# Optimization experiments

Hardware: AMD Instinct MI355X
Metric: run time of the kernel (lower is better)

## Reference

```python
import jax, jax.numpy as jnp
import numpy as np

EMB = 1024
HEAD = 128

def setup_inputs() -> dict:
    key = jax.random.key(0)
    ks = jax.random.split(key, 7)
    B, S = 4, 4096
    x = jax.random.normal(ks[0], (B, S, EMB), dtype=jnp.float32)
    s_in = 1.0 / np.sqrt(EMB)
    Wq = jax.random.uniform(ks[1], (EMB, HEAD), jnp.float32, -s_in, s_in)
    bq = jax.random.uniform(ks[2], (HEAD,), jnp.float32, -s_in, s_in)
    Wk = jax.random.uniform(ks[3], (EMB, HEAD), jnp.float32, -s_in, s_in)
    bk = jax.random.uniform(ks[4], (HEAD,), jnp.float32, -s_in, s_in)
    Wv = jax.random.uniform(ks[5], (EMB, HEAD), jnp.float32, -s_in, s_in)
    bv = jax.random.uniform(ks[6], (HEAD,), jnp.float32, -s_in, s_in)
    return {"decoder_sequence": x, "Wq": Wq, "bq": bq, "Wk": Wk, "bk": bk, "Wv": Wv, "bv": bv}

def reference(decoder_sequence, Wq, bq, Wk, bk, Wv, bv):
    # QKV projections: [B,S,E] @ [E,H] -> [B,S,H]
    Q = decoder_sequence @ Wq + bq
    K = decoder_sequence @ Wk + bk
    V = decoder_sequence @ Wv + bv
    S = decoder_sequence.shape[1]
    scale = 1.0 / jnp.sqrt(jnp.asarray(HEAD, Q.dtype))
    # scores [B,S,S]
    A = jnp.einsum('bid,bjd->bij', Q, K) * scale
    causal = jnp.tril(jnp.ones((S, S), dtype=bool))  # keep lower-triangular incl. diag
    A = jnp.where(causal, A, -jnp.inf)
    A = jax.nn.softmax(A, axis=-1)
    return jnp.einsum('bij,bjd->bid', A, V)
```

## Files before the change

kernel.cpp:

```cpp
#include <hip/hip_runtime.h>
#include <hip/hip_bf16.h>
#include <math.h>

#define S_LEN 4096
#define EMB   1024
#define HEAD  128

typedef short bf16x8 __attribute__((ext_vector_type(8)));
typedef short s16x4  __attribute__((ext_vector_type(4)));
typedef float f32x4  __attribute__((ext_vector_type(4)));

static __device__ __forceinline__ short f2bf(float x){
  unsigned u = __builtin_bit_cast(unsigned, x);
  u += 0x7fffu + ((u >> 16) & 1u);
  return (short)(u >> 16);
}
static __device__ __forceinline__ float bf2f(short s){
  unsigned u = ((unsigned)(unsigned short)s) << 16;
  return __builtin_bit_cast(float, u);
}
static __device__ __forceinline__ f32x4 mfma16(bf16x8 a, bf16x8 b, f32x4 c){
  return __builtin_amdgcn_mfma_f32_16x16x32_bf16(a, b, c, 0, 0, 0);
}
static __device__ __forceinline__ void gload16(const void* g, void* l){
  __builtin_amdgcn_global_load_lds((const __attribute__((address_space(1))) unsigned*)g,
                                   (__attribute__((address_space(3))) unsigned*)l, 16, 0, 0);
}

__global__ void prep_w(const float* __restrict__ Wq, const float* __restrict__ bq,
                       const float* __restrict__ Wk, const float* __restrict__ bk,
                       const float* __restrict__ Wv, const float* __restrict__ bv,
                       short* __restrict__ WT, float* __restrict__ bias){
  int idx = blockIdx.x * 256 + threadIdx.x;
  int nc  = idx >> 10;
  int k   = idx & 1023;
  int mat = nc >> 7;
  int n   = nc & 127;
  const float* W = (mat == 0) ? Wq : (mat == 1) ? Wk : Wv;
  float s = (mat == 0) ? 0.08838834764831845f : 1.0f;
  WT[idx] = f2bf(W[k * HEAD + n] * s);
  if (idx < 384){
    int m2 = idx >> 7, n2 = idx & 127;
    const float* bsrc = (m2 == 0) ? bq : (m2 == 1) ? bk : bv;
    float s2 = (m2 == 0) ? 0.08838834764831845f : 1.0f;
    bias[idx] = bsrc[n2] * s2;
  }
}

__global__ __launch_bounds__(1024) void qkv_proj(const float* __restrict__ x,
    const short* __restrict__ WT, const float* __restrict__ bias,
    short* __restrict__ Qo, short* __restrict__ Ko, short* __restrict__ VTo){
  __shared__ __align__(16) short Sm[2][32768];

  const int tid = threadIdx.x;
  const int wave = tid >> 6, lane = tid & 63, lr = lane & 15, hg = lane >> 4;
  const int wrg = wave >> 3, cg = wave & 7, fbase = cg * 3;
  const int row0 = blockIdx.x * 64;

  const f32x4 zero = {0.f, 0.f, 0.f, 0.f};
  f32x4 acc[2][3];
  #pragma unroll
  for (int rf = 0; rf < 2; ++rf)
    #pragma unroll
    for (int f = 0; f < 3; ++f) acc[rf][f] = zero;

#define WL(buf) (&Sm[buf][0])
#define XL(buf) ((float*)&Sm[buf][24576])

#define QKV_STAGE(buf, k0)                                                         \
  {                                                                                \
    _Pragma("unroll")                                                              \
    for (int s = 0; s < 3; ++s){                                                   \
      int slot = s * 16 + wave;                                                    \
      int ff = slot >> 1, ks = slot & 1;                                           \
      gload16(WT + (size_t)(ff * 16 + lr) * 1024 + (k0) + ks * 32 + hg * 8,        \
              WL(buf) + slot * 512);                                               \
    }                                                                              \
    {                                                                              \
      int rr = wave * 4 + hg;                                                      \
      int cs = lr ^ (rr & 15);                                                     \
      gload16(x + (size_t)(row0 + rr) * 1024 + (k0) + cs * 4,                      \
              XL(buf) + wave * 256);                                               \
    }                                                                              \
  }

  QKV_STAGE(0, 0)

  int cur = 0;
  for (int t = 0; t < 16; ++t){
    if (t < 15){
      QKV_STAGE(cur ^ 1, (t + 1) * 64)
      asm volatile("s_waitcnt vmcnt(4)" ::: "memory");
    } else {
      asm volatile("s_waitcnt vmcnt(0)" ::: "memory");
    }
    __builtin_amdgcn_s_barrier();
    asm volatile("" ::: "memory");

    bf16x8 a[2][2];
    #pragma unroll
    for (int rf = 0; rf < 2; ++rf){
      const int xr = wrg * 32 + rf * 16 + lr;
      #pragma unroll
      for (int ks = 0; ks < 2; ++ks){
        int s0 = ks * 8 + hg * 2;
        f32x4 xa = *(const f32x4*)&XL(cur)[xr * 64 + ((s0 ^ lr) << 2)];
        f32x4 xb = *(const f32x4*)&XL(cur)[xr * 64 + (((s0 + 1) ^ lr) << 2)];
        a[rf][ks][0] = f2bf(xa[0]); a[rf][ks][1] = f2bf(xa[1]);
        a[rf][ks][2] = f2bf(xa[2]); a[rf][ks][3] = f2bf(xa[3]);
        a[rf][ks][4] = f2bf(xb[0]); a[rf][ks][5] = f2bf(xb[1]);
        a[rf][ks][6] = f2bf(xb[2]); a[rf][ks][7] = f2bf(xb[3]);
      }
    }
    __builtin_amdgcn_s_setprio(1);
    #pragma unroll
    for (int fi = 0; fi < 3; ++fi){
      #pragma unroll
      for (int ks = 0; ks < 2; ++ks){
        bf16x8 bfr = *(const bf16x8*)&WL(cur)[((fbase + fi) * 2 + ks) * 512 + lane * 8];
        acc[0][fi] = mfma16(a[0][ks], bfr, acc[0][fi]);
        acc[1][fi] = mfma16(a[1][ks], bfr, acc[1][fi]);
      }
    }
    __builtin_amdgcn_s_setprio(0);
    asm volatile("" ::: "memory");
    __builtin_amdgcn_s_barrier();
    cur ^= 1;
  }

  short* Vb = &Sm[0][0];
  #pragma unroll
  for (int rf = 0; rf < 2; ++rf){
    #pragma unroll
    for (int fi = 0; fi < 3; ++fi){
      int f = fbase + fi;
      float bb = bias[f * 16 + lr];
      int rloc = wrg * 32 + rf * 16 + hg * 4;
      if (f < 16){
        short* dst = (f < 8) ? Qo : Ko;
        int col = (f & 7) * 16 + lr;
        #pragma unroll
        for (int r = 0; r < 4; ++r)
          dst[(size_t)(row0 + rloc + r) * HEAD + col] = f2bf(acc[rf][fi][r] + bb);
      } else {
        int vcol = (f - 16) * 16 + lr;
        #pragma unroll
        for (int r = 0; r < 4; ++r)
          Vb[vcol * 72 + rloc + r] = f2bf(acc[rf][fi][r] + bb);
      }
    }
  }
  __syncthreads();
  {
    int vcol = tid >> 3, sq = tid & 7;
    bf16x8 v = *(const bf16x8*)&Vb[vcol * 72 + sq * 8];
    int bb2 = row0 >> 12, ss = row0 & 4095;
    *(bf16x8*)(VTo + ((size_t)(bb2 * HEAD + vcol)) * S_LEN + ss + sq * 8) = v;
  }
}

#define PPS 36

__global__ __launch_bounds__(128, 2) void attn(const short* __restrict__ Q,
    const short* __restrict__ K, const short* __restrict__ VT,
    short* __restrict__ Opart, float* __restrict__ ML){
  __shared__ __align__(16) short Kl[2][4096];
  __shared__ __align__(16) short Vl[2][4096];
  __shared__ __align__(16) short Pl[2][2][16 * PPS];

  const int tid = threadIdx.x;
  const int wave = tid >> 6, lane = tid & 63, lr = lane & 15, hg = lane >> 4;
  const int b = blockIdx.x;
  const int i = blockIdx.y;

  int t, c;
  if (i < 232){
    c = 0;
    #pragma unroll
    for (int j = 1; j < 8; ++j) if (i >= j * (61 - 4 * j)) c = j;
    t = 8 * c + 7 + (i - c * (61 - 4 * c));
  } else {
    int p = i - 232;
    t = p + p / 7;
    c = t >> 3;
  }

  const int qt0  = t * 64;
  const int kvlo = c << 9;
  const int kvhi = min(kvlo + 512, qt0 + 64);
  const int ns   = (kvhi - kvlo) >> 5;

  const short* Qg = Q  + ((size_t)b * S_LEN + qt0 + wave * 32) * HEAD;
  const short* Kg = K  + (size_t)b * S_LEN * HEAD;
  const short* Vg = VT + (size_t)b * HEAD * S_LEN;

  bf16x8 qf[2][4];
  #pragma unroll
  for (int qs = 0; qs < 2; ++qs)
    #pragma unroll
    for (int sl = 0; sl < 4; ++sl)
      qf[qs][sl] = *(const bf16x8*)(Qg + (size_t)(qs * 16 + lr) * HEAD + sl * 32 + hg * 8);

#define ATTN_STAGE(buf, j0)                                                        \
  {                                                                                \
    if (wave == 0){                                                                \
      _Pragma("unroll")                                                            \
      for (int s = 0; s < 8; ++s)                                                  \
        gload16(Kg + (size_t)((j0) + (s >> 2) * 16 + lr) * HEAD + (s & 3) * 32 + hg * 8, \
                &Kl[buf][s * 512]);                                                \
    } else {                                                                       \
      _Pragma("unroll")                                                            \
      for (int s = 0; s < 8; ++s)                                                  \
        gload16(Vg + (size_t)(s * 16 + lr) * S_LEN + (j0) + hg * 8,                \
                &Vl[buf][s * 512]);                                                \
    }                                                                              \
  }

  ATTN_STAGE(0, kvlo)

  const f32x4 zero = {0.f, 0.f, 0.f, 0.f};
  f32x4 acc[8][2];
  #pragma unroll
  for (int f = 0; f < 8; ++f){ acc[f][0] = zero; acc[f][1] = zero; }
  float mloc[2] = {-INFINITY, -INFINITY};
  float den[2]  = {0.f, 0.f};

  int cur = 0;
  for (int st = 0; st < ns; ++st){
    const int j0 = kvlo + st * 32;
    if (st + 1 < ns){
      ATTN_STAGE(cur ^ 1, j0 + 32)
      asm volatile("s_waitcnt vmcnt(8)" ::: "memory");
    } else {
      asm volatile("s_waitcnt vmcnt(0)" ::: "memory");
    }
    __builtin_amdgcn_s_barrier();
    asm volatile("" ::: "memory");

    f32x4 sc[2][2];
    __builtin_amdgcn_s_setprio(1);
    #pragma unroll
    for (int kvs = 0; kvs < 2; ++kvs){
      sc[kvs][0] = zero; sc[kvs][1] = zero;
      #pragma unroll
      for (int sl = 0; sl < 4; ++sl){
        bf16x8 kf = *(const bf16x8*)&Kl[cur][(kvs * 4 + sl) * 512 + lane * 8];
        sc[kvs][0] = mfma16(kf, qf[0][sl], sc[kvs][0]);
        sc[kvs][1] = mfma16(kf, qf[1][sl], sc[kvs][1]);
      }
    }
    __builtin_amdgcn_s_setprio(0);

    if (j0 + 31 > qt0 + wave * 32){
      #pragma unroll
      for (int qs = 0; qs < 2; ++qs){
        int qr0 = qt0 + wave * 32 + qs * 16;
        #pragma unroll
        for (int kvs = 0; kvs < 2; ++kvs){
          int kv0 = j0 + kvs * 16 + hg * 4;
          #pragma unroll
          for (int r = 0; r < 4; ++r)
            if (kv0 + r > qr0 + lr) sc[kvs][qs][r] = -INFINITY;
        }
      }
    }

    float pm[2];
    #pragma unroll
    for (int qs = 0; qs < 2; ++qs){
      pm[qs] = fmaxf(fmaxf(fmaxf(sc[0][qs][0], sc[0][qs][1]), fmaxf(sc[0][qs][2], sc[0][qs][3])),
                     fmaxf(fmaxf(sc[1][qs][0], sc[1][qs][1]), fmaxf(sc[1][qs][2], sc[1][qs][3])));
      pm[qs] = fmaxf(pm[qs], __shfl_xor(pm[qs], 16));
      pm[qs] = fmaxf(pm[qs], __shfl_xor(pm[qs], 32));
    }

    if (__any(fmaxf(pm[0] - mloc[0], pm[1] - mloc[1]) > 8.0f)){
      #pragma unroll
      for (int qs = 0; qs < 2; ++qs){
        float mn = fmaxf(mloc[qs], pm[qs]);
        float al = __expf(mloc[qs] - mn);
        mloc[qs] = mn; den[qs] *= al;
        #pragma unroll
        for (int f = 0; f < 8; ++f) acc[f][qs] *= al;
      }
    }

    bf16x8 pf[2];
    #pragma unroll
    for (int qs = 0; qs < 2; ++qs){
      float rs = 0.f;
      s16x4 pb0, pb1;
      #pragma unroll
      for (int r = 0; r < 4; ++r){
        float p0 = __expf(sc[0][qs][r] - mloc[qs]);
        float p1 = __expf(sc[1][qs][r] - mloc[qs]);
        rs += p0 + p1;
        pb0[r] = f2bf(p0); pb1[r] = f2bf(p1);
      }
      rs += __shfl_xor(rs, 16);
      rs += __shfl_xor(rs, 32);
      den[qs] += rs;
      short* Pw = &Pl[wave][qs][0];
      *(s16x4*)(&Pw[lr * PPS + hg * 4])      = pb0;
      *(s16x4*)(&Pw[lr * PPS + 16 + hg * 4]) = pb1;
      pf[qs] = *(const bf16x8*)(&Pw[lr * PPS + hg * 8]);
    }

    __builtin_amdgcn_s_setprio(1);
    #pragma unroll
    for (int f = 0; f < 8; ++f){
      bf16x8 vf = *(const bf16x8*)&Vl[cur][f * 512 + lane * 8];
      acc[f][0] = mfma16(vf, pf[0], acc[f][0]);
      acc[f][1] = mfma16(vf, pf[1], acc[f][1]);
    }
    __builtin_amdgcn_s_setprio(0);

    asm volatile("" ::: "memory");
    __builtin_amdgcn_s_barrier();
    cur ^= 1;
  }

  const int pidx = b * 288 + i;
  short* Op = Opart + (size_t)pidx * 8192;
  #pragma unroll
  for (int qs = 0; qs < 2; ++qs){
    const float inv = 1.0f / den[qs];
    const int rowblk = wave * 2 + qs;
    #pragma unroll
    for (int f = 0; f < 8; ++f){
      s16x4 ov;
      #pragma unroll
      for (int r = 0; r < 4; ++r) ov[r] = f2bf(acc[f][qs][r] * inv);
      *(s16x4*)(Op + (rowblk * 16 + lr) * 128 + f * 16 + hg * 4) = ov;
    }
    if (hg == 0){
      ML[pidx * 128 + rowblk * 16 + lr]      = mloc[qs];
      ML[pidx * 128 + 64 + rowblk * 16 + lr] = den[qs];
    }
  }
}

__global__ __launch_bounds__(512) void combine(const short* __restrict__ Opart,
    const float* __restrict__ ML, float* __restrict__ out){
  const int t = blockIdx.x, b = blockIdx.y;
  const int row = threadIdx.x >> 3;
  const int cgp = threadIdx.x & 7;
  const int nc = (t >> 3) + 1;
  const int nheavy = (t + 1) >> 3;

  float M = -INFINITY;
  for (int cc = 0; cc < nc; ++cc){
    int ii = (cc < nheavy) ? cc * (61 - 4 * cc) + t - (8 * cc + 7)
                           : 232 + t - (t >> 3);
    M = fmaxf(M, ML[(b * 288 + ii) * 128 + row]);
  }
  float L = 0.f;
  float o[16];
  #pragma unroll
  for (int e = 0; e < 16; ++e) o[e] = 0.f;
  for (int cc = 0; cc < nc; ++cc){
    int ii = (cc < nheavy) ? cc * (61 - 4 * cc) + t - (8 * cc + 7)
                           : 232 + t - (t >> 3);
    int id = b * 288 + ii;
    float mc = ML[id * 128 + row];
    float lc = ML[id * 128 + 64 + row];
    float w = __expf(mc - M) * lc;
    L += w;
    const short* op = Opart + (size_t)id * 8192 + row * 128 + cgp * 16;
    bf16x8 v0 = *(const bf16x8*)(op);
    bf16x8 v1 = *(const bf16x8*)(op + 8);
    #pragma unroll
    for (int e = 0; e < 8; ++e){
      o[e]     += w * bf2f(v0[e]);
      o[8 + e] += w * bf2f(v1[e]);
    }
  }
  float inv = 1.f / L;
  float* dst = out + ((size_t)b * S_LEN + t * 64 + row) * HEAD + cgp * 16;
  #pragma unroll
  for (int e4 = 0; e4 < 4; ++e4){
    float4 w4 = { o[e4*4]*inv, o[e4*4+1]*inv, o[e4*4+2]*inv, o[e4*4+3]*inv };
    *(float4*)(dst + e4 * 4) = w4;
  }
}

extern "C" void kernel_launch(void* const* d_in, const int* in_sizes, int n_in,
                              void* d_out, int out_size, void* d_ws, size_t ws_size,
                              hipStream_t stream){
  const float* x  = (const float*)d_in[0];
  const float* Wq = (const float*)d_in[1];
  const float* bq = (const float*)d_in[2];
  const float* Wk = (const float*)d_in[3];
  const float* bk = (const float*)d_in[4];
  const float* Wv = (const float*)d_in[5];
  const float* bv = (const float*)d_in[6];
  float* out = (float*)d_out;

  char* ws = (char*)d_ws;
  short* WT    = (short*)(ws);
  float* bias  = (float*)(ws + 786432);
  short* Qb    = (short*)(ws + (1u << 20));
  short* Kb    = (short*)(ws + (1u << 20) + 4194304u);
  short* VTb   = (short*)(ws + (1u << 20) + 8388608u);
  short* Opart = (short*)(ws + 13631488u);
  float* ML    = (float*)(ws + 32505856u);

  prep_w<<<1536, 256, 0, stream>>>(Wq, bq, Wk, bk, Wv, bv, WT, bias);
  qkv_proj<<<256, 1024, 0, stream>>>(x, WT, bias, Qb, Kb, VTb);
  attn<<<dim3(4, 288), 128, 0, stream>>>(Qb, Kb, VTb, Opart, ML);
  combine<<<dim3(64, 4), 512, 0, stream>>>(Opart, ML, out);
}
```

Before: 105.4 us.

## Enlarge attention blocks to eight waves over 256-row query tiles

The attention kernel moves from 2-wave blocks covering 64 query rows to 8-wave blocks covering 256 query rows. All eight waves now share each staged K/V tile, and every wave issues one K load and one V load per stage. The split-KV work map is rebuilt around 512-key chunks with half-length diagonal blocks, and the partial-output layout and the combine kernel are re-indexed to match. This cuts global-to-LDS traffic per unit of work. The cost is far fewer blocks (288 on a 256-CU part) with uneven lengths, and coarser causal tiles that compute more masked entries on the diagonal.

```diff
diff --git a/kernel.cpp b/kernel.cpp
--- a/kernel.cpp
+++ b/kernel.cpp
@@ -161,34 +161,35 @@
 
 #define PPS 36
 
-__global__ __launch_bounds__(128, 2) void attn(const short* __restrict__ Q,
+__global__ __launch_bounds__(512) void attn(const short* __restrict__ Q,
     const short* __restrict__ K, const short* __restrict__ VT,
     short* __restrict__ Opart, float* __restrict__ ML){
   __shared__ __align__(16) short Kl[2][4096];
   __shared__ __align__(16) short Vl[2][4096];
-  __shared__ __align__(16) short Pl[2][2][16 * PPS];
+  __shared__ __align__(16) short Pl[8][16 * PPS];
 
   const int tid = threadIdx.x;
   const int wave = tid >> 6, lane = tid & 63, lr = lane & 15, hg = lane >> 4;
   const int b = blockIdx.x;
   const int i = blockIdx.y;
 
-  int t, c;
-  if (i < 232){
-    c = 0;
-    #pragma unroll
-    for (int j = 1; j < 8; ++j) if (i >= j * (61 - 4 * j)) c = j;
-    t = 8 * c + 7 + (i - c * (61 - 4 * c));
+  int t, c, full;
+  if (i < 64){
+    int acc = 0; t = 0; c = 0;
+    #pragma unroll
+    for (int tt = 0; tt < 16; ++tt){
+      int nf = (tt & 1) ? (tt >> 1) + 1 : (tt >> 1);
+      if (i >= acc && i < acc + nf){ t = tt; c = i - acc; }
+      acc += nf;
+    }
+    full = 1;
   } else {
-    int p = i - 232;
-    t = p + p / 7;
-    c = t >> 3;
-  }
-
-  const int qt0  = t * 64;
+    int k = i - 64; t = 2 * k; c = k; full = 0;
+  }
+
+  const int qt0  = t * 256;
   const int kvlo = c << 9;
-  const int kvhi = min(kvlo + 512, qt0 + 64);
-  const int ns   = (kvhi - kvlo) >> 5;
+  const int ns   = full ? 16 : 8;
 
   const short* Qg = Q  + ((size_t)b * S_LEN + qt0 + wave * 32) * HEAD;
   const short* Kg = K  + (size_t)b * S_LEN * HEAD;
@@ -203,17 +204,10 @@
 
 #define ATTN_STAGE(buf, j0)                                                        \
   {                                                                                \
-    if (wave == 0){                                                                \
-      _Pragma("unroll")                                                            \
-      for (int s = 0; s < 8; ++s)                                                  \
-        gload16(Kg + (size_t)((j0) + (s >> 2) * 16 + lr) * HEAD + (s & 3) * 32 + hg * 8, \
-                &Kl[buf][s * 512]);                                                \
-    } else {                                                                       \
-      _Pragma("unroll")                                                            \
-      for (int s = 0; s < 8; ++s)                                                  \
-        gload16(Vg + (size_t)(s * 16 + lr) * S_LEN + (j0) + hg * 8,                \
-                &Vl[buf][s * 512]);                                                \
-    }                                                                              \
+    gload16(Kg + (size_t)((j0) + (wave >> 2) * 16 + lr) * HEAD + (wave & 3) * 32 + hg * 8, \
+            &Kl[buf][wave * 512]);                                                 \
+    gload16(Vg + (size_t)(wave * 16 + lr) * S_LEN + (j0) + hg * 8,                 \
+            &Vl[buf][wave * 512]);                                                 \
   }
 
   ATTN_STAGE(0, kvlo)
@@ -230,7 +224,7 @@
     const int j0 = kvlo + st * 32;
     if (st + 1 < ns){
       ATTN_STAGE(cur ^ 1, j0 + 32)
-      asm volatile("s_waitcnt vmcnt(8)" ::: "memory");
+      asm volatile("s_waitcnt vmcnt(2)" ::: "memory");
     } else {
       asm volatile("s_waitcnt vmcnt(0)" ::: "memory");
     }
@@ -286,6 +280,7 @@
     }
 
     bf16x8 pf[2];
+    short* Pw = &Pl[wave][0];
     #pragma unroll
     for (int qs = 0; qs < 2; ++qs){
       float rs = 0.f;
@@ -300,7 +295,6 @@
       rs += __shfl_xor(rs, 16);
       rs += __shfl_xor(rs, 32);
       den[qs] += rs;
-      short* Pw = &Pl[wave][qs][0];
       *(s16x4*)(&Pw[lr * PPS + hg * 4])      = pb0;
       *(s16x4*)(&Pw[lr * PPS + 16 + hg * 4]) = pb1;
       pf[qs] = *(const bf16x8*)(&Pw[lr * PPS + hg * 8]);
@@ -320,53 +314,55 @@
     cur ^= 1;
   }
 
-  const int pidx = b * 288 + i;
-  short* Op = Opart + (size_t)pidx * 8192;
+  const int pidx = b * 72 + i;
+  short* Op = Opart + (size_t)pidx * 32768;
   #pragma unroll
   for (int qs = 0; qs < 2; ++qs){
     const float inv = 1.0f / den[qs];
-    const int rowblk = wave * 2 + qs;
+    const int rI = wave * 32 + qs * 16 + lr;
     #pragma unroll
     for (int f = 0; f < 8; ++f){
       s16x4 ov;
       #pragma unroll
       for (int r = 0; r < 4; ++r) ov[r] = f2bf(acc[f][qs][r] * inv);
-      *(s16x4*)(Op + (rowblk * 16 + lr) * 128 + f * 16 + hg * 4) = ov;
+      *(s16x4*)(Op + rI * 128 + f * 16 + hg * 4) = ov;
     }
     if (hg == 0){
-      ML[pidx * 128 + rowblk * 16 + lr]      = mloc[qs];
-      ML[pidx * 128 + 64 + rowblk * 16 + lr] = den[qs];
+      ML[pidx * 512 + rI]       = mloc[qs];
+      ML[pidx * 512 + 256 + rI] = den[qs];
     }
   }
 }
 
 __global__ __launch_bounds__(512) void combine(const short* __restrict__ Opart,
     const float* __restrict__ ML, float* __restrict__ out){
-  const int t = blockIdx.x, b = blockIdx.y;
+  const int bx = blockIdx.x, b = blockIdx.y;
+  const int t = bx >> 2, sub = bx & 3;
   const int row = threadIdx.x >> 3;
   const int cgp = threadIdx.x & 7;
-  const int nc = (t >> 3) + 1;
-  const int nheavy = (t + 1) >> 3;
+  const int rI = sub * 64 + row;
+  const int k = t >> 1;
+  const int F = k * k + ((t & 1) ? k : 0);
+  const int nf = (t & 1) ? k + 1 : k;
+  const int nc = k + 1;
 
   float M = -INFINITY;
   for (int cc = 0; cc < nc; ++cc){
-    int ii = (cc < nheavy) ? cc * (61 - 4 * cc) + t - (8 * cc + 7)
-                           : 232 + t - (t >> 3);
-    M = fmaxf(M, ML[(b * 288 + ii) * 128 + row]);
+    int ii = (cc < nf) ? F + cc : 64 + k;
+    M = fmaxf(M, ML[(b * 72 + ii) * 512 + rI]);
   }
   float L = 0.f;
   float o[16];
   #pragma unroll
   for (int e = 0; e < 16; ++e) o[e] = 0.f;
   for (int cc = 0; cc < nc; ++cc){
-    int ii = (cc < nheavy) ? cc * (61 - 4 * cc) + t - (8 * cc + 7)
-                           : 232 + t - (t >> 3);
-    int id = b * 288 + ii;
-    float mc = ML[id * 128 + row];
-    float lc = ML[id * 128 + 64 + row];
+    int ii = (cc < nf) ? F + cc : 64 + k;
+    int id = b * 72 + ii;
+    float mc = ML[id * 512 + rI];
+    float lc = ML[id * 512 + 256 + rI];
     float w = __expf(mc - M) * lc;
     L += w;
-    const short* op = Opart + (size_t)id * 8192 + row * 128 + cgp * 16;
+    const short* op = Opart + (size_t)id * 32768 + rI * 128 + cgp * 16;
     bf16x8 v0 = *(const bf16x8*)(op);
     bf16x8 v1 = *(const bf16x8*)(op + 8);
     #pragma unroll
@@ -376,7 +372,7 @@
     }
   }
   float inv = 1.f / L;
-  float* dst = out + ((size_t)b * S_LEN + t * 64 + row) * HEAD + cgp * 16;
+  float* dst = out + ((size_t)b * S_LEN + t * 256 + rI) * HEAD + cgp * 16;
   #pragma unroll
   for (int e4 = 0; e4 < 4; ++e4){
     float4 w4 = { o[e4*4]*inv, o[e4*4+1]*inv, o[e4*4+2]*inv, o[e4*4+3]*inv };
@@ -407,6 +403,6 @@
 
   prep_w<<<1536, 256, 0, stream>>>(Wq, bq, Wk, bk, Wv, bv, WT, bias);
   qkv_proj<<<256, 1024, 0, stream>>>(x, WT, bias, Qb, Kb, VTb);
-  attn<<<dim3(4, 288), 128, 0, stream>>>(Qb, Kb, VTb, Opart, ML);
+  attn<<<dim3(4, 72), 512, 0, stream>>>(Qb, Kb, VTb, Opart, ML);
   combine<<<dim3(64, 4), 512, 0, stream>>>(Opart, ML, out);
 }
```

Measured after the change: 112.6 us. 6.9% more time.
